# Kernel optimization log

Hardware: AMD Instinct MI355X
Metric: run time of the kernel (lower is better)

## Reference

```python
import jax, jax.numpy as jnp
import numpy as np

B, C, T = 16, 768, 1024
STEPS, NNEG, OFFSET = 12, 10, 1
COPIES = NNEG + 1


def setup_inputs() -> dict:
    key = jax.random.key(0)
    k1, k2, k3, k4 = jax.random.split(key, 4)
    x = jax.random.normal(k1, (B, C, T), jnp.float32)
    y = jax.random.normal(k2, (B, C, T), jnp.float32)
    # ConvTranspose2d(in_dim, out_dim, (1, steps)) weight -> [C_in, C_out, steps]
    W = jax.random.normal(k3, (C, C, STEPS), jnp.float32) * 0.02
    b = jnp.zeros((C,), jnp.float32)
    # Negative-sample indices, replicating torch sample_negatives (sample_distance=None):
    # randint in [0, T-1), bump collisions with the positive timestep, add per-batch offset.
    neg = jax.random.randint(k4, (B, NNEG * T), 0, T - 1)
    tszs = jnp.repeat(jnp.arange(T), NNEG)  # [NNEG*T]
    neg = jnp.where(neg >= tszs[None, :], neg + 1, neg)
    neg = neg + jnp.arange(B)[:, None] * T  # index into flattened [B*T]
    return {"x": x, "y": y, "W": W, "b": b, "neg_idxs": neg}


def reference(x, y, W, b, neg_idxs):
    # project_to_steps: ConvTranspose2d with kernel (1, STEPS) on [B,C,T,1] -> [B,C,T,STEPS]
    proj = jnp.einsum('bct,cds->bdts', x, W) + b[None, :, None, None]

    # gather negatives: y -> [C, B*T], fancy-index, reshape to [NNEG, B, C, T]
    yf = jnp.transpose(y, (1, 0, 2)).reshape(C, B * T)
    negs = yf[:, neg_idxs.reshape(-1)].reshape(C, B, NNEG, T)
    negs = jnp.transpose(negs, (2, 1, 0, 3))  # [NNEG, B, C, T]

    targets = jnp.concatenate([y[None], negs], axis=0)  # [COPIES, B, C, T]

    steps = min(STEPS, T - OFFSET)
    preds = []
    for i in range(steps):  # small fixed loop over prediction steps (ragged slice sizes)
        off = i + OFFSET
        # [T-off, B, COPIES]: dot context at step i with targets shifted by off
        p = jnp.einsum('bct,nbct->tbn', proj[..., :T - off, i], targets[..., off:])
        preds.append(p.reshape(-1))
    predictions = jnp.concatenate(preds).reshape(-1, COPIES)  # infonce logits
    labels = jnp.zeros((predictions.shape[0],), jnp.int32)  # positive is copy 0
    return predictions, labels
```

## Files before the change

kernel.cpp:

```cpp
#include <hip/hip_runtime.h>

typedef __bf16 bf16;
typedef __attribute__((ext_vector_type(8))) __bf16 bf16x8;
typedef __attribute__((ext_vector_type(4))) __bf16 bf16x4;
typedef __attribute__((ext_vector_type(4))) float f32x4;

#define B_ 16
#define C_ 768
#define T_ 1024
#define S_ 12
#define TP_ (T_ + S_)
#define NNEG_ 10
#define NCOPY 11
#define NPRED_ROWS 195360
#define NPRED (NPRED_ROWS * NCOPY)
#define NT_ 12
#define TC_ 512

__device__ __forceinline__ void gload16(const void* g, void* l) {
    __builtin_amdgcn_global_load_lds(
        (__attribute__((address_space(1))) void*)g,
        (__attribute__((address_space(3))) void*)l, 16, 0, 0);
}

__global__ __launch_bounds__(256) void k_wt(const float* __restrict__ W, bf16* __restrict__ WtT) {
    __shared__ float sW[32 * 385];
    const int c0 = blockIdx.x * 32, d0 = blockIdx.y * 32;
    const int tid = threadIdx.x;
#pragma unroll 4
    for (int k = 0; k < 48; ++k) {
        int idx = k * 256 + tid;
        int c = idx / 384, r = idx % 384;
        sW[c * 385 + r] = W[((size_t)(c0 + c) * C_ + d0) * S_ + r];
    }
    __syncthreads();
#pragma unroll 4
    for (int k = 0; k < 48; ++k) {
        int idx = k * 256 + tid;
        int row = idx >> 5, c = idx & 31;
        int s = row >> 5, d = row & 31;
        WtT[((size_t)s * C_ + d0 + d) * C_ + c0 + c] = (bf16)sW[c * 385 + d * 12 + s];
    }
}

__global__ void k_tr2(const float* __restrict__ x, const float* __restrict__ y,
                      bf16* __restrict__ xTc, bf16* __restrict__ yTc, int b0, int cb) {
    __shared__ float tile[32][33];
    int zz = blockIdx.z;
    const float* src = (zz < cb) ? x : y;
    bf16* dst = (zz < cb) ? xTc : yTc;
    int bb = (zz < cb) ? zz : zz - cb;
    int b = b0 + bb;
    int c0 = blockIdx.y * 32, t0 = blockIdx.x * 32;
    int tx = threadIdx.x & 31, ty = threadIdx.x >> 5;
#pragma unroll
    for (int i = 0; i < 4; ++i)
        tile[ty + i * 8][tx] = src[((size_t)b * C_ + c0 + ty + i * 8) * T_ + t0 + tx];
    __syncthreads();
#pragma unroll
    for (int i = 0; i < 4; ++i)
        dst[((size_t)bb * T_ + t0 + ty + i * 8) * C_ + c0 + tx] = (bf16)tile[tx][ty + i * 8];
}

#define SBAR()  __builtin_amdgcn_s_barrier()
#define SCHED() __builtin_amdgcn_sched_barrier(0)
#define LGKM0() asm volatile("s_waitcnt lgkmcnt(0)" ::: "memory")

__global__ __launch_bounds__(512, 2) void k_gemm8(
    const bf16* __restrict__ xTc, const bf16* __restrict__ WtT,
    const float* __restrict__ bias, bf16* __restrict__ P, int tc0)
{
    const int nblk = blockIdx.x;
    const int t0   = tc0 + blockIdx.y * 256;
    const int bb   = blockIdx.z;

    const int tid  = threadIdx.x;
    const int wv   = tid >> 6, lane = tid & 63;
    const int mwz  = wv >> 2, nwz = wv & 3;
    const int quad = lane >> 4, l15 = lane & 15;

    __shared__ __align__(16) bf16 sA[2][256][64];
    __shared__ __align__(16) bf16 sB[2][256][64];

    const int lrow = lane >> 3;
    const int laneOff = lrow * 1536 + (((lane & 7) * 16) ^ (lrow << 4));
    const char* aG = (const char*)(WtT + (size_t)(nblk * 256) * C_) + laneOff;
    const char* bG = (const char*)(xTc + ((size_t)bb * T_ + t0) * C_) + laneOff;
    const int h0 = wv * 16, h1 = wv * 16 + 8;
    const int arw0 = (h0 & 63) + ((h0 >> 6) << 7);
    const int arw1 = (h1 & 63) + ((h1 >> 6) << 7);
    const int brw0 = (h0 & 31) + ((h0 >> 5) << 6);
    const int brw1 = (h1 & 31) + ((h1 >> 5) << 6);

#define STAGE_A(bufn, roff, kt) do { \
    gload16(aG + (size_t)(arw0 + (roff)) * 1536 + (kt) * 128, &sA[bufn][arw0 + (roff)][0]); \
    gload16(aG + (size_t)(arw1 + (roff)) * 1536 + (kt) * 128, &sA[bufn][arw1 + (roff)][0]); \
} while (0)
#define STAGE_B(bufn, roff, kt) do { \
    gload16(bG + (size_t)(brw0 + (roff)) * 1536 + (kt) * 128, &sB[bufn][brw0 + (roff)][0]); \
    gload16(bG + (size_t)(brw1 + (roff)) * 1536 + (kt) * 128, &sB[bufn][brw1 + (roff)][0]); \
} while (0)

    const int csw0 = (quad * 16) ^ ((l15 & 7) << 4);
    const int csw1 = (64 + quad * 16) ^ ((l15 & 7) << 4);
    const char* aRd0 = (const char*)&sA[0][mwz * 128 + l15][0] + csw0;
    const char* aRd1 = (const char*)&sA[0][mwz * 128 + l15][0] + csw1;
    const char* bRd0 = (const char*)&sB[0][nwz * 64 + l15][0] + csw0;
    const char* bRd1 = (const char*)&sB[0][nwz * 64 + l15][0] + csw1;

    f32x4 acc[8][4] = {};

    STAGE_A(0, 0, 0);
    STAGE_A(0, 64, 0);
    STAGE_B(0, 32, 0);
    STAGE_B(0, 0, 0);
    STAGE_A(1, 0, 1);
    STAGE_B(1, 32, 1);
    STAGE_A(1, 64, 1);
    asm volatile("s_waitcnt vmcnt(6)" ::: "memory");
    SCHED(); SBAR(); SCHED();

#pragma unroll 2
    for (int j = 0; j < NT_; ++j) {
        const int cur = j & 1;
        const int coff = cur << 15;
        const char* aC0 = aRd0 + coff; const char* aC1 = aRd1 + coff;
        const char* bC0 = bRd0 + coff; const char* bC1 = bRd1 + coff;

        bf16x8 a03[4][2], a47[4][2], b01[2][2], b23[2][2], b01p[2][2];

        if (j + 1 < NT_) STAGE_B(cur ^ 1, 0, j + 1);
#pragma unroll
        for (int i = 0; i < 4; ++i) {
            a03[i][0] = *(const bf16x8*)(aC0 + i * 2048);
            a03[i][1] = *(const bf16x8*)(aC1 + i * 2048);
        }
#pragma unroll
        for (int i = 0; i < 2; ++i) {
            b01[i][0] = *(const bf16x8*)(bC0 + i * 2048);
            b01[i][1] = *(const bf16x8*)(bC1 + i * 2048);
        }
        SCHED(); SBAR(); LGKM0(); SCHED();
        __builtin_amdgcn_s_setprio(1);
#pragma unroll
        for (int i = 0; i < 4; ++i)
#pragma unroll
            for (int n = 0; n < 2; ++n)
#pragma unroll
                for (int kk = 0; kk < 2; ++kk)
                    acc[i][n] = __builtin_amdgcn_mfma_f32_16x16x32_bf16(a03[i][kk], b01[n][kk], acc[i][n], 0, 0, 0);
        __builtin_amdgcn_s_setprio(0);
        SCHED(); SBAR(); SCHED();

        if (j + 2 < NT_) STAGE_A(cur, 0, j + 2);
#pragma unroll
        for (int i = 0; i < 2; ++i) {
            b23[i][0] = *(const bf16x8*)(bC0 + 4096 + i * 2048);
            b23[i][1] = *(const bf16x8*)(bC1 + 4096 + i * 2048);
        }
        SCHED(); SBAR(); LGKM0(); SCHED();
        __builtin_amdgcn_s_setprio(1);
#pragma unroll
        for (int i = 0; i < 4; ++i)
#pragma unroll
            for (int n = 0; n < 2; ++n)
#pragma unroll
                for (int kk = 0; kk < 2; ++kk)
                    acc[i][2 + n] = __builtin_amdgcn_mfma_f32_16x16x32_bf16(a03[i][kk], b23[n][kk], acc[i][2 + n], 0, 0, 0);
        __builtin_amdgcn_s_setprio(0);
        SCHED(); SBAR(); SCHED();

        if (j + 2 < NT_) STAGE_B(cur, 32, j + 2);
#pragma unroll
        for (int i = 0; i < 4; ++i) {
            a47[i][0] = *(const bf16x8*)(aC0 + 8192 + i * 2048);
            a47[i][1] = *(const bf16x8*)(aC1 + 8192 + i * 2048);
        }
        SCHED(); SBAR(); LGKM0(); SCHED();
        __builtin_amdgcn_s_setprio(1);
#pragma unroll
        for (int i = 0; i < 4; ++i)
#pragma unroll
            for (int n = 0; n < 2; ++n)
#pragma unroll
                for (int kk = 0; kk < 2; ++kk)
                    acc[4 + i][2 + n] = __builtin_amdgcn_mfma_f32_16x16x32_bf16(a47[i][kk], b23[n][kk], acc[4 + i][2 + n], 0, 0, 0);
        __builtin_amdgcn_s_setprio(0);
        SCHED(); SBAR(); SCHED();

        if (j + 2 < NT_) STAGE_A(cur, 64, j + 2);
#pragma unroll
        for (int i = 0; i < 2; ++i) {
            b01p[i][0] = *(const bf16x8*)(bC0 + i * 2048);
            b01p[i][1] = *(const bf16x8*)(bC1 + i * 2048);
        }
        if (j < NT_ - 2)       { asm volatile("s_waitcnt vmcnt(6)" ::: "memory"); }
        else if (j == NT_ - 2) { asm volatile("s_waitcnt vmcnt(0)" ::: "memory"); }
        SCHED(); SBAR(); LGKM0(); SCHED();
        __builtin_amdgcn_s_setprio(1);
#pragma unroll
        for (int i = 0; i < 4; ++i)
#pragma unroll
            for (int n = 0; n < 2; ++n)
#pragma unroll
                for (int kk = 0; kk < 2; ++kk)
                    acc[4 + i][n] = __builtin_amdgcn_mfma_f32_16x16x32_bf16(a47[i][kk], b01p[n][kk], acc[4 + i][n], 0, 0, 0);
        __builtin_amdgcn_s_setprio(0);
        SCHED(); SBAR(); SCHED();
    }

    const size_t SC = (size_t)S_ * C_;
    const int sblk = nblk / 3;
    const int dblk = (nblk % 3) * 256;
    bf16* Pb = P + (size_t)bb * TP_ * SC + (size_t)sblk * C_ + dblk;
#pragma unroll
    for (int i = 0; i < 8; ++i) {
        const int nloc = mwz * 128 + i * 16 + quad * 4;
        const f32x4 bv = *(const f32x4*)&bias[dblk + nloc];
#pragma unroll
        for (int n = 0; n < 4; ++n) {
            const int t = t0 + nwz * 64 + n * 16 + l15;
            const int tp = t + sblk + 1;
            bf16x4 v;
#pragma unroll
            for (int r = 0; r < 4; ++r) v[r] = (bf16)(acc[i][n][r] + bv[r]);
            *(bf16x4*)&Pb[(size_t)tp * SC + nloc] = v;
        }
    }
#undef STAGE_A
#undef STAGE_B
}

__global__ __launch_bounds__(256, 4) void k_pred(
    const bf16* __restrict__ P, const bf16* __restrict__ yTc,
    const int* __restrict__ neg, float* __restrict__ out, int b0, int tp0, int cb)
{
    const int widx = blockIdx.x;
    const int bb = widx % cb;
    const int tp = tp0 + widx / cb;
    if (tp > T_ - 1) return;
    const int b = b0 + bb;
    const int tid = threadIdx.x;

    __shared__ __align__(16) char sAB[24 * 1536];
    __shared__ int sRid[12];

    if (tid < 12) {
        int ridx;
        if (tid == 0) ridx = bb * T_ + tp;
        else ridx = neg[(size_t)b * (NNEG_ * T_) + (tid - 1) * T_ + tp] - b0 * T_;
        sRid[tid] = ridx;
    }
    __syncthreads();

    const char* Prow = (const char*)(P + ((size_t)bb * TP_ + tp) * (S_ * C_));
#pragma unroll
    for (int i = 0; i < 18; ++i) {
        int idx = i * 256 + tid;
        int row = idx / 192;
        int off = (idx % 192) * 8;
        unsigned long long v;
        if (row < 12) {
            v = *(const unsigned long long*)(Prow + idx * 8);
        } else {
            v = *(const unsigned long long*)((const char*)(yTc + (size_t)sRid[row - 12] * C_) + off);
        }
        int sb = ((off & ~15) ^ ((row & 7) << 4)) | (off & 8);
        *(unsigned long long*)(&sAB[row * 1536 + sb]) = v;
    }
    __syncthreads();

    const int wv = tid >> 6, lane = tid & 63;
    const int quad = lane >> 4, l15 = lane & 15;

    const int ra = l15 < 12 ? l15 : 11;
    const int rb = 12 + (l15 < 12 ? l15 : 11);
    const char* pa = sAB + ra * 1536;
    const char* pb = sAB + rb * 1536;
    const int xa = (ra & 7) << 4, xb = (rb & 7) << 4;

    f32x4 acc = {};
#pragma unroll
    for (int k = 0; k < 6; ++k) {
        const int kt = wv * 6 + k;
        const int col = ((kt << 2) + quad) << 4;
        bf16x8 av = *(const bf16x8*)(pa + (col ^ xa));
        bf16x8 bv = *(const bf16x8*)(pb + (col ^ xb));
        acc = __builtin_amdgcn_mfma_f32_16x16x32_bf16(av, bv, acc, 0, 0, 0);
    }

    __syncthreads();
    if (wv > 0) *(f32x4*)&sAB[wv * 1024 + lane * 16] = acc;
    __syncthreads();
    if (wv > 0) return;

#pragma unroll
    for (int w = 1; w < 4; ++w) {
        const f32x4 p = *(const f32x4*)&sAB[w * 1024 + lane * 16];
#pragma unroll
        for (int r = 0; r < 4; ++r) acc[r] += p[r];
    }

#pragma unroll
    for (int r = 0; r < 4; ++r) {
        int s = quad * 4 + r;
        int t = tp - 1 - s;
        if (s < S_ && t >= 0) {
            int rowbase = s * (T_ - 1) - (s * (s - 1)) / 2;
            size_t row = (size_t)(rowbase + t) * B_ + b;
            if (l15 < NCOPY)       out[row * NCOPY + l15] = acc[r];
            else if (l15 == NCOPY) out[NPRED + row] = 0.0f;
        }
    }
}

extern "C" void kernel_launch(void* const* d_in, const int* in_sizes, int n_in,
                              void* d_out, int out_size, void* d_ws, size_t ws_size,
                              hipStream_t stream) {
    const float* x    = (const float*)d_in[0];
    const float* y    = (const float*)d_in[1];
    const float* W    = (const float*)d_in[2];
    const float* bias = (const float*)d_in[3];
    const int*   neg  = (const int*)d_in[4];
    float* out = (float*)d_out;

    const size_t offW    = (size_t)S_ * C_ * C_ * 2;
    const size_t perb_xy = (size_t)T_ * C_ * 2;
    const size_t perb_p  = (size_t)TP_ * S_ * C_ * 2;
    const size_t perb    = 2 * perb_xy + perb_p;

    int bchunk = (int)((ws_size - offW) / perb);
    if (bchunk < 1) bchunk = 1;
    if (bchunk > B_) bchunk = B_;

    char* ws = (char*)d_ws;
    bf16* WtT = (bf16*)ws;
    bf16* xTc = (bf16*)(ws + offW);
    bf16* yTc = (bf16*)(ws + offW + (size_t)bchunk * perb_xy);
    bf16* P   = (bf16*)(ws + offW + (size_t)bchunk * perb_xy * 2);

    k_wt<<<dim3(C_ / 32, C_ / 32), 256, 0, stream>>>(W, WtT);

    for (int b0 = 0; b0 < B_;) {
        int cb = bchunk < (B_ - b0) ? bchunk : (B_ - b0);
        k_tr2<<<dim3(T_ / 32, C_ / 32, 2 * cb), 256, 0, stream>>>(x, y, xTc, yTc, b0, cb);
        for (int tc = 0; tc < T_; tc += TC_) {
            k_gemm8<<<dim3(36, TC_ / 256, cb), 512, 0, stream>>>(xTc, WtT, bias, P, tc);
            k_pred<<<dim3(cb << 9), 256, 0, stream>>>(P, yTc, neg, out, b0, tc + 1, cb);
        }
        b0 += cb;
    }
}
```

Baseline: 692.1 us.

## Simplify GEMM pipeline to two phases and launch full-T grids once

Restructures the k_gemm8 main loop from four MFMA phases with interleaved partial stages to two phases. Each phase loads all four B fragments once and reuses them for both A halves, with a single barrier-gated prefetch of the next tile. The host also stops splitting T into two chunks and launches gemm and pred once per batch chunk over the full T range, halving launch count and giving larger grids. The new pipeline issues dummy loads of tile 0 on the final iterations, and its vmcnt accounting differs from before, which may change how well load latency is overlapped.

```diff
diff --git a/kernel.cpp b/kernel.cpp
--- a/kernel.cpp
+++ b/kernel.cpp
@@ -15,7 +15,6 @@
 #define NPRED_ROWS 195360
 #define NPRED (NPRED_ROWS * NCOPY)
 #define NT_ 12
-#define TC_ 512
 
 __device__ __forceinline__ void gload16(const void* g, void* l) {
     __builtin_amdgcn_global_load_lds(
@@ -68,10 +67,10 @@
 
 __global__ __launch_bounds__(512, 2) void k_gemm8(
     const bf16* __restrict__ xTc, const bf16* __restrict__ WtT,
-    const float* __restrict__ bias, bf16* __restrict__ P, int tc0)
+    const float* __restrict__ bias, bf16* __restrict__ P)
 {
     const int nblk = blockIdx.x;
-    const int t0   = tc0 + blockIdx.y * 256;
+    const int t0   = blockIdx.y * 256;
     const int bb   = blockIdx.z;
 
     const int tid  = threadIdx.x;
@@ -111,14 +110,10 @@
     f32x4 acc[8][4] = {};
 
     STAGE_A(0, 0, 0);
+    STAGE_B(0, 0, 0);
+    STAGE_B(0, 32, 0);
     STAGE_A(0, 64, 0);
-    STAGE_B(0, 32, 0);
-    STAGE_B(0, 0, 0);
     STAGE_A(1, 0, 1);
-    STAGE_B(1, 32, 1);
-    STAGE_A(1, 64, 1);
-    asm volatile("s_waitcnt vmcnt(6)" ::: "memory");
-    SCHED(); SBAR(); SCHED();
 
 #pragma unroll 2
     for (int j = 0; j < NT_; ++j) {
@@ -126,88 +121,57 @@
         const int coff = cur << 15;
         const char* aC0 = aRd0 + coff; const char* aC1 = aRd1 + coff;
         const char* bC0 = bRd0 + coff; const char* bC1 = bRd1 + coff;
-
-        bf16x8 a03[4][2], a47[4][2], b01[2][2], b23[2][2], b01p[2][2];
-
-        if (j + 1 < NT_) STAGE_B(cur ^ 1, 0, j + 1);
+        const int kt1 = (j + 1 < NT_) ? j + 1 : 0;
+        const int kt2 = (j + 2 < NT_) ? j + 2 : 0;
+
+        bf16x8 a03[4][2], a47[4][2], bfr[4][2];
+
+        STAGE_B(cur ^ 1, 0, kt1);
+        STAGE_B(cur ^ 1, 32, kt1);
+        STAGE_A(cur ^ 1, 64, kt1);
+        asm volatile("s_waitcnt vmcnt(8)" ::: "memory");
+        SCHED(); SBAR(); SCHED();
 #pragma unroll
         for (int i = 0; i < 4; ++i) {
             a03[i][0] = *(const bf16x8*)(aC0 + i * 2048);
             a03[i][1] = *(const bf16x8*)(aC1 + i * 2048);
         }
 #pragma unroll
-        for (int i = 0; i < 2; ++i) {
-            b01[i][0] = *(const bf16x8*)(bC0 + i * 2048);
-            b01[i][1] = *(const bf16x8*)(bC1 + i * 2048);
-        }
-        SCHED(); SBAR(); LGKM0(); SCHED();
+        for (int n = 0; n < 4; ++n) {
+            bfr[n][0] = *(const bf16x8*)(bC0 + n * 2048);
+            bfr[n][1] = *(const bf16x8*)(bC1 + n * 2048);
+        }
+        LGKM0(); SCHED();
         __builtin_amdgcn_s_setprio(1);
 #pragma unroll
         for (int i = 0; i < 4; ++i)
 #pragma unroll
-            for (int n = 0; n < 2; ++n)
+            for (int n = 0; n < 4; ++n)
 #pragma unroll
                 for (int kk = 0; kk < 2; ++kk)
-                    acc[i][n] = __builtin_amdgcn_mfma_f32_16x16x32_bf16(a03[i][kk], b01[n][kk], acc[i][n], 0, 0, 0);
+                    acc[i][n] = __builtin_amdgcn_mfma_f32_16x16x32_bf16(a03[i][kk], bfr[n][kk], acc[i][n], 0, 0, 0);
         __builtin_amdgcn_s_setprio(0);
         SCHED(); SBAR(); SCHED();
 
-        if (j + 2 < NT_) STAGE_A(cur, 0, j + 2);
-#pragma unroll
-        for (int i = 0; i < 2; ++i) {
-            b23[i][0] = *(const bf16x8*)(bC0 + 4096 + i * 2048);
-            b23[i][1] = *(const bf16x8*)(bC1 + 4096 + i * 2048);
-        }
-        SCHED(); SBAR(); LGKM0(); SCHED();
-        __builtin_amdgcn_s_setprio(1);
-#pragma unroll
-        for (int i = 0; i < 4; ++i)
-#pragma unroll
-            for (int n = 0; n < 2; ++n)
-#pragma unroll
-                for (int kk = 0; kk < 2; ++kk)
-                    acc[i][2 + n] = __builtin_amdgcn_mfma_f32_16x16x32_bf16(a03[i][kk], b23[n][kk], acc[i][2 + n], 0, 0, 0);
-        __builtin_amdgcn_s_setprio(0);
-        SCHED(); SBAR(); SCHED();
-
-        if (j + 2 < NT_) STAGE_B(cur, 32, j + 2);
+        STAGE_A(cur, 0, kt2);
 #pragma unroll
         for (int i = 0; i < 4; ++i) {
             a47[i][0] = *(const bf16x8*)(aC0 + 8192 + i * 2048);
             a47[i][1] = *(const bf16x8*)(aC1 + 8192 + i * 2048);
         }
-        SCHED(); SBAR(); LGKM0(); SCHED();
+        LGKM0(); SCHED();
         __builtin_amdgcn_s_setprio(1);
 #pragma unroll
         for (int i = 0; i < 4; ++i)
 #pragma unroll
-            for (int n = 0; n < 2; ++n)
+            for (int n = 0; n < 4; ++n)
 #pragma unroll
                 for (int kk = 0; kk < 2; ++kk)
-                    acc[4 + i][2 + n] = __builtin_amdgcn_mfma_f32_16x16x32_bf16(a47[i][kk], b23[n][kk], acc[4 + i][2 + n], 0, 0, 0);
+                    acc[4 + i][n] = __builtin_amdgcn_mfma_f32_16x16x32_bf16(a47[i][kk], bfr[n][kk], acc[4 + i][n], 0, 0, 0);
         __builtin_amdgcn_s_setprio(0);
         SCHED(); SBAR(); SCHED();
-
-        if (j + 2 < NT_) STAGE_A(cur, 64, j + 2);
-#pragma unroll
-        for (int i = 0; i < 2; ++i) {
-            b01p[i][0] = *(const bf16x8*)(bC0 + i * 2048);
-            b01p[i][1] = *(const bf16x8*)(bC1 + i * 2048);
-        }
-        if (j < NT_ - 2)       { asm volatile("s_waitcnt vmcnt(6)" ::: "memory"); }
-        else if (j == NT_ - 2) { asm volatile("s_waitcnt vmcnt(0)" ::: "memory"); }
-        SCHED(); SBAR(); LGKM0(); SCHED();
-        __builtin_amdgcn_s_setprio(1);
-#pragma unroll
-        for (int i = 0; i < 4; ++i)
-#pragma unroll
-            for (int n = 0; n < 2; ++n)
-#pragma unroll
-                for (int kk = 0; kk < 2; ++kk)
-                    acc[4 + i][n] = __builtin_amdgcn_mfma_f32_16x16x32_bf16(a47[i][kk], b01p[n][kk], acc[4 + i][n], 0, 0, 0);
-        __builtin_amdgcn_s_setprio(0);
-        SCHED(); SBAR(); SCHED();
-    }
+    }
+    asm volatile("s_waitcnt vmcnt(0)" ::: "memory");
 
     const size_t SC = (size_t)S_ * C_;
     const int sblk = nblk / 3;
@@ -344,10 +308,8 @@
     for (int b0 = 0; b0 < B_;) {
         int cb = bchunk < (B_ - b0) ? bchunk : (B_ - b0);
         k_tr2<<<dim3(T_ / 32, C_ / 32, 2 * cb), 256, 0, stream>>>(x, y, xTc, yTc, b0, cb);
-        for (int tc = 0; tc < T_; tc += TC_) {
-            k_gemm8<<<dim3(36, TC_ / 256, cb), 512, 0, stream>>>(xTc, WtT, bias, P, tc);
-            k_pred<<<dim3(cb << 9), 256, 0, stream>>>(P, yTc, neg, out, b0, tc + 1, cb);
-        }
+        k_gemm8<<<dim3(36, 4, cb), 512, 0, stream>>>(xTc, WtT, bias, P);
+        k_pred<<<dim3(cb * 1023), 256, 0, stream>>>(P, yTc, neg, out, b0, 1, cb);
         b0 += cb;
     }
 }
```

Result: faster. 604.2 us (-12.7%).
